# Kernel optimization log

Measured on AMD Instinct MI355X. Metric: run time of the kernel, lower is better.

Reference implementation:

```python
import jax, jax.numpy as jnp
import numpy as np

N_NODES = 100000
N_EDGES = 1600000
IN_CH = 128
HID = 32
HEADS = 4
OUT_CH = 32
NEG_SLOPE = 0.2  # PyG GATConv default


def setup_inputs() -> dict:
    key = jax.random.key(0)
    ks = jax.random.split(key, 12)
    s = 0.1
    x = jax.random.normal(ks[0], (N_NODES, IN_CH), dtype=jnp.float32)
    edge_index = jax.random.randint(ks[1], (2, N_EDGES), 0, N_NODES, dtype=jnp.int64)
    # layer 1: in -> heads*hid, concat
    W1 = jax.random.normal(ks[2], (IN_CH, HEADS * HID), dtype=jnp.float32) * s
    a_src1 = jax.random.normal(ks[3], (HEADS, HID), dtype=jnp.float32) * s
    a_dst1 = jax.random.normal(ks[4], (HEADS, HID), dtype=jnp.float32) * s
    b1 = jnp.zeros((HEADS * HID,), dtype=jnp.float32)
    # layer 2: heads*hid -> out, single head, averaged
    W2 = jax.random.normal(ks[5], (HEADS * HID, OUT_CH), dtype=jnp.float32) * s
    a_src2 = jax.random.normal(ks[6], (1, OUT_CH), dtype=jnp.float32) * s
    a_dst2 = jax.random.normal(ks[7], (1, OUT_CH), dtype=jnp.float32) * s
    b2 = jnp.zeros((OUT_CH,), dtype=jnp.float32)
    return {"x": x, "edge_index": edge_index, "W1": W1, "a_src1": a_src1,
            "a_dst1": a_dst1, "b1": b1, "W2": W2, "a_src2": a_src2,
            "a_dst2": a_dst2, "b2": b2}


def _gat_layer(x, src, dst, W, a_s, a_d, b, heads, ch, concat):
    n = x.shape[0]
    h = (x @ W).reshape(n, heads, ch)            # [N,H,C]
    alpha_s = jnp.einsum('nhc,hc->nh', h, a_s)   # [N,H]
    alpha_d = jnp.einsum('nhc,hc->nh', h, a_d)
    e = jax.nn.leaky_relu(alpha_s[src] + alpha_d[dst], NEG_SLOPE)  # [E,H]
    # segment softmax over edges sharing a destination (self-loops guarantee
    # every segment is non-empty)
    m = jax.ops.segment_max(e, dst, num_segments=n)
    ex = jnp.exp(e - m[dst])
    denom = jax.ops.segment_sum(ex, dst, num_segments=n)
    alpha = ex / (denom[dst] + 1e-16)            # [E,H]
    out = jax.ops.segment_sum(alpha[:, :, None] * h[src], dst, num_segments=n)  # [N,H,C]
    out = out.reshape(n, heads * ch) if concat else out.mean(axis=1)
    return out + b


def reference(x, edge_index, W1, a_src1, a_dst1, b1, W2, a_src2, a_dst2, b2):
    n = x.shape[0]
    loop = jnp.arange(n, dtype=edge_index.dtype)
    src = jnp.concatenate([edge_index[0], loop])  # add self-loops (PyG default)
    dst = jnp.concatenate([edge_index[1], loop])
    h = _gat_layer(x, src, dst, W1, a_src1, a_dst1, b1, HEADS, HID, True)
    h = jax.nn.relu(h)
    # dropout(p=0.5) is identity in eval mode
    out = _gat_layer(h, src, dst, W2, a_src2, a_dst2, b2, 1, OUT_CH, False)
    return out
```

## Files before the change

kernel.cpp:

```cpp
#include <hip/hip_runtime.h>
#include <math.h>

#define NEG_SLOPE 0.2f
#define EPB 8192

typedef __attribute__((ext_vector_type(8))) short bf16x8;
typedef __attribute__((ext_vector_type(4))) float f32x4;

__device__ __forceinline__ unsigned pack_bf16x2(float a, float b) {
    unsigned ua = __float_as_uint(a);
    unsigned ub = __float_as_uint(b);
    ua += 0x7FFFu + ((ua >> 16) & 1u);
    ub += 0x7FFFu + ((ub >> 16) & 1u);
    return (ua >> 16) | (ub & 0xFFFF0000u);
}
__device__ __forceinline__ unsigned short bf16r(float f) {
    unsigned u = __float_as_uint(f);
    u += 0x7FFFu + ((u >> 16) & 1u);
    return (unsigned short)(u >> 16);
}
__device__ __forceinline__ float bf_lo(unsigned u) { return __uint_as_float(u << 16); }
__device__ __forceinline__ float bf_hi(unsigned u) { return __uint_as_float(u & 0xFFFF0000u); }

#define SWZ(row, byteoff) ((((row) * 256) + (byteoff)) ^ (((row) & 15) << 4))


__global__ __launch_bounds__(256) void wcvt_kernel(const float* __restrict__ W,
                                                   unsigned short* __restrict__ WT,
                                                   int Nc, int total) {
    int id = blockIdx.x * 256 + threadIdx.x;
    if (id < total) {
        int n = id >> 7, k = id & 127;
        WT[id] = bf16r(W[k * Nc + n]);
    }
}


__global__ __launch_bounds__(256) void gscan_bsum(const int* __restrict__ arr,
                                                  int* __restrict__ psum, int M) {
    __shared__ int red[4];
    int tid = threadIdx.x;
    int idx = blockIdx.x * 256 + tid;
    int v = (idx < M) ? arr[idx] : 0;
    #pragma unroll
    for (int off = 1; off < 64; off <<= 1) v += __shfl_xor(v, off, 64);
    if ((tid & 63) == 0) red[tid >> 6] = v;
    __syncthreads();
    if (tid == 0) psum[blockIdx.x] = red[0] + red[1] + red[2] + red[3];
}

__global__ __launch_bounds__(1024) void gscan_psum(int* __restrict__ psum, int nb) {
    __shared__ int ws[16];
    int tid = threadIdx.x, lane = tid & 63, w = tid >> 6;
    int v = (tid < nb) ? psum[tid] : 0;
    int incl = v;
    #pragma unroll
    for (int off = 1; off < 64; off <<= 1) {
        int t = __shfl_up(incl, off, 64);
        if (lane >= off) incl += t;
    }
    if (lane == 63) ws[w] = incl;
    __syncthreads();
    int wbase = 0;
    #pragma unroll
    for (int j = 0; j < 16; j++) { if (j < w) wbase += ws[j]; }
    if (tid < nb) psum[tid] = wbase + incl - v;
}

__global__ __launch_bounds__(256) void gscan_final(int* __restrict__ arr,
                                                   const int* __restrict__ psum, int M) {
    __shared__ int ws[4];
    int tid = threadIdx.x, lane = tid & 63, w = tid >> 6;
    int idx = blockIdx.x * 256 + tid;
    int v = (idx < M) ? arr[idx] : 0;
    int incl = v;
    #pragma unroll
    for (int off = 1; off < 64; off <<= 1) {
        int t = __shfl_up(incl, off, 64);
        if (lane >= off) incl += t;
    }
    if (lane == 63) ws[w] = incl;
    __syncthreads();
    int wbase = 0;
    #pragma unroll
    for (int j = 0; j < 4; j++) { if (j < w) wbase += ws[j]; }
    if (idx < M) arr[idx] = psum[blockIdx.x] + wbase + incl - v;
}


__global__ __launch_bounds__(256) void p1_hist(const int* __restrict__ dst, int E, int N,
                                               int nblk1, int nbuckets,
                                               int* __restrict__ partial) {
    __shared__ int hist[1024];
    int tid = threadIdx.x;
    for (int i = tid; i < nbuckets; i += 256) hist[i] = 0;
    __syncthreads();
    int base = blockIdx.x * EPB;
    int tot = E + N;
    #pragma unroll
    for (int it = 0; it < EPB / 256; it++) {
        int i = base + it * 256 + tid;
        if (i < tot) {
            int d = (i < E) ? dst[i] : (i - E);
            atomicAdd(&hist[d >> 8], 1);
        }
    }
    __syncthreads();
    for (int b = tid; b < nbuckets; b += 256)
        partial[b * nblk1 + blockIdx.x] = hist[b];
}

__global__ __launch_bounds__(256) void p1_scatter(const int* __restrict__ src,
                                                  const int* __restrict__ dst, int E, int N,
                                                  int nblk1, int nbuckets,
                                                  const int* __restrict__ scanned,
                                                  unsigned* __restrict__ pairs) {
    __shared__ int cursor[1024];
    int tid = threadIdx.x;
    for (int b = tid; b < nbuckets; b += 256)
        cursor[b] = scanned[b * nblk1 + blockIdx.x];
    __syncthreads();
    int base = blockIdx.x * EPB;
    int tot = E + N;
    #pragma unroll
    for (int it = 0; it < EPB / 256; it++) {
        int i = base + it * 256 + tid;
        if (i < tot) {
            int s = (i < E) ? src[i] : (i - E);
            int d = (i < E) ? dst[i] : (i - E);
            int pos = atomicAdd(&cursor[d >> 8], 1);
            pairs[pos] = ((unsigned)(d & 255) << 24) | (unsigned)s;
        }
    }
}

#define P2CAP 8192

__global__ __launch_bounds__(256) void p2_kernel(const unsigned* __restrict__ pairs,
                                                 const int* __restrict__ scanned,
                                                 int nblk1, int nbuckets, int Etot, int N,
                                                 int* __restrict__ rowptr,
                                                 int* __restrict__ col) {
    __shared__ unsigned buf[P2CAP];
    __shared__ int cnt[256];
    __shared__ int cur[256];
    __shared__ int wsum[4];
    int b = blockIdx.x;
    int tid = threadIdx.x, lane = tid & 63, w = tid >> 6;
    int bucketStart = scanned[b * nblk1];
    int bucketEnd = (b + 1 < nbuckets) ? scanned[(b + 1) * nblk1] : Etot;
    int sz = bucketEnd - bucketStart;
    bool inLds = (sz <= P2CAP);
    cnt[tid] = 0;
    if (inLds) {
        for (int i = tid; i < sz; i += 256) buf[i] = pairs[bucketStart + i];
    }
    __syncthreads();
    if (inLds) {
        for (int i = tid; i < sz; i += 256) atomicAdd(&cnt[buf[i] >> 24], 1);
    } else {
        for (int i = bucketStart + tid; i < bucketEnd; i += 256)
            atomicAdd(&cnt[pairs[i] >> 24], 1);
    }
    __syncthreads();
    int v = cnt[tid];
    int incl = v;
    #pragma unroll
    for (int off = 1; off < 64; off <<= 1) {
        int t = __shfl_up(incl, off, 64);
        if (lane >= off) incl += t;
    }
    if (lane == 63) wsum[w] = incl;
    __syncthreads();
    int wbase = 0;
    #pragma unroll
    for (int j = 0; j < 4; j++) { if (j < w) wbase += wsum[j]; }
    int base = bucketStart + wbase + incl - v;
    cur[tid] = base;
    int d = b * 256 + tid;
    if (d < N) rowptr[d] = base;
    if (b == nbuckets - 1 && tid == 0) rowptr[N] = Etot;
    __syncthreads();
    if (inLds) {
        for (int i = tid; i < sz; i += 256) {
            unsigned p = buf[i];
            int pos = atomicAdd(&cur[p >> 24], 1);
            col[pos] = (int)(p & 0xFFFFFFu);
        }
    } else {
        for (int i = bucketStart + tid; i < bucketEnd; i += 256) {
            unsigned p = pairs[i];
            int pos = atomicAdd(&cur[p >> 24], 1);
            col[pos] = (int)(p & 0xFFFFFFu);
        }
    }
}


__global__ __launch_bounds__(256) void gemm1_kernel(const float* __restrict__ x,
                                                    const unsigned short* __restrict__ W1T,
                                                    const float* __restrict__ a_s,
                                                    const float* __restrict__ a_d,
                                                    uint4* __restrict__ h1b,
                                                    float* __restrict__ as1,
                                                    float* __restrict__ ad1, int N) {
    __shared__ char xs[16384];
    __shared__ char wsm[32768];
    int tid = threadIdx.x;
    int row0 = blockIdx.x * 64;

    #pragma unroll
    for (int it = 0; it < 8; it++) {
        int idx = it * 256 + tid;
        int n = idx >> 4, kq = idx & 15;
        uint4 v = ((const uint4*)W1T)[idx];
        *(uint4*)(wsm + SWZ(n, kq * 16)) = v;
    }
    #pragma unroll
    for (int it = 0; it < 8; it++) {
        int idx = it * 256 + tid;
        int r = idx >> 5, k4 = idx & 31;
        int row = row0 + r;
        float4 v = (row < N) ? ((const float4*)x)[(size_t)row * 32 + k4]
                             : make_float4(0.f, 0.f, 0.f, 0.f);
        uint2 p;
        p.x = pack_bf16x2(v.x, v.y);
        p.y = pack_bf16x2(v.z, v.w);
        *(uint2*)(xs + SWZ(r, k4 * 8)) = p;
    }
    __syncthreads();

    int wv = tid >> 6, lane = tid & 63;
    int r0 = wv * 16;
    int lm = lane & 15, lk = lane >> 4;

    bf16x8 afr[4];
    #pragma unroll
    for (int ks = 0; ks < 4; ks++) {
        int row = r0 + lm;
        afr[ks] = *(const bf16x8*)(xs + SWZ(row, ks * 64 + lk * 16));
    }
    f32x4 acc[8];
    #pragma unroll
    for (int nt = 0; nt < 8; nt++) acc[nt] = (f32x4){0.f, 0.f, 0.f, 0.f};

    #pragma unroll
    for (int nt = 0; nt < 8; nt++) {
        int c = nt * 16 + lm;
        #pragma unroll
        for (int ks = 0; ks < 4; ks++) {
            bf16x8 bfr = *(const bf16x8*)(wsm + SWZ(c, ks * 64 + lk * 16));
            acc[nt] = __builtin_amdgcn_mfma_f32_16x16x32_bf16(afr[ks], bfr, acc[nt], 0, 0, 0);
        }
    }
    __syncthreads();

    #pragma unroll
    for (int nt = 0; nt < 8; nt++) {
        int c = nt * 16 + lm;
        #pragma unroll
        for (int e = 0; e < 4; e++) {
            int row = r0 + lk * 4 + e;
            *(unsigned short*)(xs + SWZ(row, c * 2)) = bf16r(acc[nt][e]);
        }
    }
    __syncthreads();

    #pragma unroll
    for (int it = 0; it < 4; it++) {
        int idx = it * 256 + tid;
        int row = idx >> 4, q = idx & 15;
        if (row0 + row < N) {
            uint4 v = *(const uint4*)(xs + SWZ(row, q * 16));
            h1b[(size_t)(row0 + row) * 16 + q] = v;
        }
    }
    {
        int row = tid >> 2, h = tid & 3;
        if (row0 + row < N) {
            float sd = 0.f, dd = 0.f;
            #pragma unroll
            for (int q = 0; q < 4; q++) {
                uint4 v = *(const uint4*)(xs + SWZ(row, h * 64 + q * 16));
                unsigned uu[4] = {v.x, v.y, v.z, v.w};
                #pragma unroll
                for (int j = 0; j < 4; j++) {
                    int k = h * 32 + q * 8 + 2 * j;
                    sd = fmaf(bf_lo(uu[j]), a_s[k], sd);
                    sd = fmaf(bf_hi(uu[j]), a_s[k + 1], sd);
                    dd = fmaf(bf_lo(uu[j]), a_d[k], dd);
                    dd = fmaf(bf_hi(uu[j]), a_d[k + 1], dd);
                }
            }
            as1[(row0 + row) * 4 + h] = sd;
            ad1[(row0 + row) * 4 + h] = dd;
        }
    }
}


__global__ __launch_bounds__(256) void agg1_kernel(const int* __restrict__ rowptr,
                                                   const int* __restrict__ col,
                                                   const unsigned* __restrict__ h1b,
                                                   const float* __restrict__ as1,
                                                   const float* __restrict__ ad1,
                                                   const float* __restrict__ b1,
                                                   unsigned* __restrict__ out1b, int N) {
    int lane = threadIdx.x & 63;
    int wid = __builtin_amdgcn_readfirstlane(threadIdx.x >> 6);
    int n = blockIdx.x * 4 + wid;
    if (n >= N) return;
    int hh = lane >> 4;
    float adn = ad1[n * 4 + hh];
    int beg = rowptr[n], end = rowptr[n + 1];
    float ax0 = 0.f, ay0 = 0.f, den0 = 0.f;
    float ax1 = 0.f, ay1 = 0.f, den1 = 0.f;
    int i = beg;
    for (; i + 16 <= end; i += 16) {
        int ss[16];
        float ll[16];
        unsigned uu[16];
        #pragma unroll
        for (int j = 0; j < 16; j++) ss[j] = col[i + j];
        #pragma unroll
        for (int j = 0; j < 16; j++) {
            ll[j] = as1[ss[j] * 4 + hh];
            uu[j] = h1b[ss[j] * 64 + lane];
        }
        #pragma unroll
        for (int j = 0; j < 16; j++) {
            float e = ll[j] + adn;
            e = fmaxf(e, e * NEG_SLOPE);
            float ex = __expf(e);
            if (j & 1) {
                den1 += ex;
                ax1 = fmaf(ex, bf_lo(uu[j]), ax1);
                ay1 = fmaf(ex, bf_hi(uu[j]), ay1);
            } else {
                den0 += ex;
                ax0 = fmaf(ex, bf_lo(uu[j]), ax0);
                ay0 = fmaf(ex, bf_hi(uu[j]), ay0);
            }
        }
    }
    for (; i + 4 <= end; i += 4) {
        int ss[4];
        float ll[4];
        unsigned uu[4];
        #pragma unroll
        for (int j = 0; j < 4; j++) ss[j] = col[i + j];
        #pragma unroll
        for (int j = 0; j < 4; j++) {
            ll[j] = as1[ss[j] * 4 + hh];
            uu[j] = h1b[ss[j] * 64 + lane];
        }
        #pragma unroll
        for (int j = 0; j < 4; j++) {
            float e = ll[j] + adn;
            e = fmaxf(e, e * NEG_SLOPE);
            float ex = __expf(e);
            den0 += ex;
            ax0 = fmaf(ex, bf_lo(uu[j]), ax0);
            ay0 = fmaf(ex, bf_hi(uu[j]), ay0);
        }
    }
    for (; i < end; i++) {
        int s = col[i];
        float l = as1[s * 4 + hh];
        unsigned u = h1b[s * 64 + lane];
        float e = l + adn;
        e = fmaxf(e, e * NEG_SLOPE);
        float ex = __expf(e);
        den0 += ex;
        ax0 = fmaf(ex, bf_lo(u), ax0);
        ay0 = fmaf(ex, bf_hi(u), ay0);
    }
    float den = den0 + den1, ax = ax0 + ax1, ay = ay0 + ay1;
    float2 bb = ((const float2*)b1)[lane];
    float ox = fmaxf(ax / den + bb.x, 0.f);
    float oy = fmaxf(ay / den + bb.y, 0.f);
    out1b[n * 64 + lane] = pack_bf16x2(ox, oy);
}


__global__ __launch_bounds__(256) void gemm2_kernel(const uint4* __restrict__ out1b,
                                                    const unsigned short* __restrict__ W2T,
                                                    const float* __restrict__ a_s,
                                                    const float* __restrict__ a_d,
                                                    uint4* __restrict__ h2b,
                                                    float* __restrict__ as2,
                                                    float* __restrict__ ad2, int N) {
    __shared__ char xs[16384];
    __shared__ char wsm[8192];
    int tid = threadIdx.x;
    int row0 = blockIdx.x * 64;

    #pragma unroll
    for (int it = 0; it < 2; it++) {
        int idx = it * 256 + tid;
        int n = idx >> 4, kq = idx & 15;
        uint4 v = ((const uint4*)W2T)[idx];
        *(uint4*)(wsm + SWZ(n, kq * 16)) = v;
    }
    #pragma unroll
    for (int it = 0; it < 4; it++) {
        int idx = it * 256 + tid;
        int r = idx >> 4, q = idx & 15;
        int row = row0 + r;
        uint4 v = (row < N) ? out1b[(size_t)row * 16 + q] : make_uint4(0, 0, 0, 0);
        *(uint4*)(xs + SWZ(r, q * 16)) = v;
    }
    __syncthreads();

    int wv = tid >> 6, lane = tid & 63;
    int r0 = wv * 16;
    int lm = lane & 15, lk = lane >> 4;

    bf16x8 afr[4];
    #pragma unroll
    for (int ks = 0; ks < 4; ks++) {
        int row = r0 + lm;
        afr[ks] = *(const bf16x8*)(xs + SWZ(row, ks * 64 + lk * 16));
    }
    f32x4 acc[2];
    acc[0] = (f32x4){0.f, 0.f, 0.f, 0.f};
    acc[1] = (f32x4){0.f, 0.f, 0.f, 0.f};
    #pragma unroll
    for (int nt = 0; nt < 2; nt++) {
        int c = nt * 16 + lm;
        #pragma unroll
        for (int ks = 0; ks < 4; ks++) {
            bf16x8 bfr = *(const bf16x8*)(wsm + SWZ(c, ks * 64 + lk * 16));
            acc[nt] = __builtin_amdgcn_mfma_f32_16x16x32_bf16(afr[ks], bfr, acc[nt], 0, 0, 0);
        }
    }
    __syncthreads();

    #pragma unroll
    for (int nt = 0; nt < 2; nt++) {
        int c = nt * 16 + lm;
        #pragma unroll
        for (int e = 0; e < 4; e++) {
            int row = r0 + lk * 4 + e;
            *(unsigned short*)(xs + SWZ(row, c * 2)) = bf16r(acc[nt][e]);
        }
    }
    __syncthreads();

    {
        int row = tid >> 2, q = tid & 3;
        if (row0 + row < N) {
            uint4 v = *(const uint4*)(xs + SWZ(row, q * 16));
            h2b[(size_t)(row0 + row) * 4 + q] = v;
        }
    }
    if (tid < 64 && row0 + tid < N) {
        float sd = 0.f, dd = 0.f;
        #pragma unroll
        for (int q = 0; q < 4; q++) {
            uint4 v = *(const uint4*)(xs + SWZ(tid, q * 16));
            unsigned uu[4] = {v.x, v.y, v.z, v.w};
            #pragma unroll
            for (int j = 0; j < 4; j++) {
                int k = q * 8 + 2 * j;
                sd = fmaf(bf_lo(uu[j]), a_s[k], sd);
                sd = fmaf(bf_hi(uu[j]), a_s[k + 1], sd);
                dd = fmaf(bf_lo(uu[j]), a_d[k], dd);
                dd = fmaf(bf_hi(uu[j]), a_d[k + 1], dd);
            }
        }
        as2[row0 + tid] = sd;
        ad2[row0 + tid] = dd;
    }
}


#define AGG2_EDGE(u, l)                                            \
    {                                                              \
        float e = l + adn;                                         \
        e = fmaxf(e, e * NEG_SLOPE);                               \
        float ex = __expf(e);                                      \
        den += ex;                                                 \
        a0 = fmaf(ex, bf_lo(u), a0);                               \
        a1 = fmaf(ex, bf_hi(u), a1);                               \
    }

__global__ __launch_bounds__(256) void agg2_kernel(const int* __restrict__ rowptr,
                                                   const int* __restrict__ col,
                                                   const unsigned* __restrict__ h2b,
                                                   const float* __restrict__ as2,
                                                   const float* __restrict__ ad2,
                                                   const float* __restrict__ b2,
                                                   float* __restrict__ out, int N) {
    int lane = threadIdx.x & 63;
    int wid = __builtin_amdgcn_readfirstlane(threadIdx.x >> 6);
    int n = blockIdx.x * 4 + wid;
    if (n >= N) return;
    int q = lane >> 4, c2 = lane & 15;
    float adn = ad2[n];
    int beg = rowptr[n], end = rowptr[n + 1];
    float a0 = 0.f, a1 = 0.f, den = 0.f;
    int i = beg;
    for (; i + 16 <= end; i += 16) {
        int s0 = col[i + q];
        int s1 = col[i + 4 + q];
        int s2 = col[i + 8 + q];
        int s3 = col[i + 12 + q];
        unsigned u0 = h2b[s0 * 16 + c2];
        unsigned u1 = h2b[s1 * 16 + c2];
        unsigned u2 = h2b[s2 * 16 + c2];
        unsigned u3 = h2b[s3 * 16 + c2];
        float l0 = as2[s0], l1 = as2[s1], l2 = as2[s2], l3 = as2[s3];
        AGG2_EDGE(u0, l0) AGG2_EDGE(u1, l1) AGG2_EDGE(u2, l2) AGG2_EDGE(u3, l3)
    }
    for (; i + 4 <= end; i += 4) {
        int s = col[i + q];
        unsigned u = h2b[s * 16 + c2];
        float l = as2[s];
        AGG2_EDGE(u, l)
    }
    if (i + q < end) {
        int s = col[i + q];
        unsigned u = h2b[s * 16 + c2];
        float l = as2[s];
        AGG2_EDGE(u, l)
    }
    den += __shfl_xor(den, 16, 64);
    den += __shfl_xor(den, 32, 64);
    a0 += __shfl_xor(a0, 16, 64);
    a0 += __shfl_xor(a0, 32, 64);
    a1 += __shfl_xor(a1, 16, 64);
    a1 += __shfl_xor(a1, 32, 64);
    if (q == 0) {
        float2 bb = ((const float2*)b2)[c2];
        ((float2*)out)[n * 16 + c2] = make_float2(a0 / den + bb.x, a1 / den + bb.y);
    }
}


extern "C" void kernel_launch(void* const* d_in, const int* in_sizes, int n_in,
                              void* d_out, int out_size, void* d_ws, size_t ws_size,
                              hipStream_t stream) {
    const float* x    = (const float*)d_in[0];
    const int*   ei   = (const int*)d_in[1];
    const float* W1   = (const float*)d_in[2];
    const float* a_s1 = (const float*)d_in[3];
    const float* a_d1 = (const float*)d_in[4];
    const float* b1   = (const float*)d_in[5];
    const float* W2   = (const float*)d_in[6];
    const float* a_s2 = (const float*)d_in[7];
    const float* a_d2 = (const float*)d_in[8];
    const float* b2   = (const float*)d_in[9];

    int N = in_sizes[0] / 128;
    int E = in_sizes[1] / 2;
    const int* srcA = ei;
    const int* dstA = ei + E;
    int Etot = E + N;

    char* ws = (char*)d_ws;
    size_t off = 0;
    auto alloc = [&](size_t bytes) {
        void* p = ws + off;
        off += (bytes + 255) & ~(size_t)255;
        return p;
    };
    unsigned* h1b   = (unsigned*)alloc((size_t)N * 128 * 2);
    unsigned* out1b = (unsigned*)alloc((size_t)N * 128 * 2);
    unsigned* h2b   = (unsigned*)alloc((size_t)N * 32 * 2);
    float* as1      = (float*)alloc((size_t)N * 4 * 4);
    float* ad1      = (float*)alloc((size_t)N * 4 * 4);
    float* as2      = (float*)alloc((size_t)N * 4);
    float* ad2      = (float*)alloc((size_t)N * 4);
    int*   rowptr   = (int*)alloc((size_t)(N + 1) * 4);
    int*   col      = (int*)alloc((size_t)Etot * 4);
    unsigned* pairs = (unsigned*)alloc((size_t)Etot * 4);
    unsigned short* W1T = (unsigned short*)alloc(128 * 128 * 2);
    unsigned short* W2T = (unsigned short*)alloc(32 * 128 * 2);

    int nbuckets = (N + 255) >> 8;
    int nblk1 = (Etot + EPB - 1) / EPB;
    int M = nbuckets * nblk1;
    int*   partial = (int*)alloc((size_t)M * 4);
    int nbs = (M + 255) / 256;
    int*   psum    = (int*)alloc((size_t)1024 * 4);

    hipLaunchKernelGGL(wcvt_kernel, dim3(64), dim3(256), 0, stream, W1, W1T, 128, 16384);
    hipLaunchKernelGGL(wcvt_kernel, dim3(16), dim3(256), 0, stream, W2, W2T, 32, 4096);

    hipLaunchKernelGGL(p1_hist, dim3(nblk1), dim3(256), 0, stream,
                       dstA, E, N, nblk1, nbuckets, partial);
    hipLaunchKernelGGL(gscan_bsum, dim3(nbs), dim3(256), 0, stream, partial, psum, M);
    hipLaunchKernelGGL(gscan_psum, dim3(1), dim3(1024), 0, stream, psum, nbs);
    hipLaunchKernelGGL(gscan_final, dim3(nbs), dim3(256), 0, stream, partial, psum, M);
    hipLaunchKernelGGL(p1_scatter, dim3(nblk1), dim3(256), 0, stream,
                       srcA, dstA, E, N, nblk1, nbuckets, partial, pairs);
    hipLaunchKernelGGL(p2_kernel, dim3(nbuckets), dim3(256), 0, stream,
                       pairs, partial, nblk1, nbuckets, Etot, N, rowptr, col);

    hipLaunchKernelGGL(gemm1_kernel, dim3((N + 63) / 64), dim3(256), 0, stream,
                       x, W1T, a_s1, a_d1, (uint4*)h1b, as1, ad1, N);
    hipLaunchKernelGGL(agg1_kernel, dim3((N + 3) / 4), dim3(256), 0, stream,
                       rowptr, col, h1b, as1, ad1, b1, out1b, N);
    hipLaunchKernelGGL(gemm2_kernel, dim3((N + 63) / 64), dim3(256), 0, stream,
                       (const uint4*)out1b, W2T, a_s2, a_d2, (uint4*)h2b, as2, ad2, N);
    hipLaunchKernelGGL(agg2_kernel, dim3((N + 3) / 4), dim3(256), 0, stream,
                       rowptr, col, h2b, as2, ad2, b2, (float*)d_out, N);
}
```

Measured before the change: 217.7 us.

## Precompute layer-1 edge attention exponentials in CSR build kernel

Moves gemm1 ahead of the CSR construction so the p2 bucket-sort kernel can compute the leaky-relu and exp of the layer-1 attention logits for all four heads per edge. It writes these into a new per-edge float4 array in CSR order. agg1 then reads the precomputed weights contiguously instead of gathering as1 by source and evaluating exp per lane. This trades a random gather plus exp in agg1 for an extra random as1 gather in p2 and roughly 27 MB of extra edge-array writes and reads.

After: 234.0 us. 7.5% more time.

```diff
diff --git a/kernel.cpp b/kernel.cpp
--- a/kernel.cpp
+++ b/kernel.cpp
@@ -139,8 +139,11 @@
 __global__ __launch_bounds__(256) void p2_kernel(const unsigned* __restrict__ pairs,
                                                  const int* __restrict__ scanned,
                                                  int nblk1, int nbuckets, int Etot, int N,
+                                                 const float4* __restrict__ as4,
+                                                 const float4* __restrict__ ad4,
                                                  int* __restrict__ rowptr,
-                                                 int* __restrict__ col) {
+                                                 int* __restrict__ col,
+                                                 float4* __restrict__ exa) {
     __shared__ unsigned buf[P2CAP];
     __shared__ int cnt[256];
     __shared__ int cur[256];
@@ -184,14 +187,34 @@
     if (inLds) {
         for (int i = tid; i < sz; i += 256) {
             unsigned p = buf[i];
-            int pos = atomicAdd(&cur[p >> 24], 1);
-            col[pos] = (int)(p & 0xFFFFFFu);
+            int dl = p >> 24, s = (int)(p & 0xFFFFFFu);
+            int pos = atomicAdd(&cur[dl], 1);
+            col[pos] = s;
+            float4 A = as4[s];
+            float4 D = ad4[b * 256 + dl];
+            float4 ex;
+            float e;
+            e = A.x + D.x; e = fmaxf(e, e * NEG_SLOPE); ex.x = __expf(e);
+            e = A.y + D.y; e = fmaxf(e, e * NEG_SLOPE); ex.y = __expf(e);
+            e = A.z + D.z; e = fmaxf(e, e * NEG_SLOPE); ex.z = __expf(e);
+            e = A.w + D.w; e = fmaxf(e, e * NEG_SLOPE); ex.w = __expf(e);
+            exa[pos] = ex;
         }
     } else {
         for (int i = bucketStart + tid; i < bucketEnd; i += 256) {
             unsigned p = pairs[i];
-            int pos = atomicAdd(&cur[p >> 24], 1);
-            col[pos] = (int)(p & 0xFFFFFFu);
+            int dl = p >> 24, s = (int)(p & 0xFFFFFFu);
+            int pos = atomicAdd(&cur[dl], 1);
+            col[pos] = s;
+            float4 A = as4[s];
+            float4 D = ad4[b * 256 + dl];
+            float4 ex;
+            float e;
+            e = A.x + D.x; e = fmaxf(e, e * NEG_SLOPE); ex.x = __expf(e);
+            e = A.y + D.y; e = fmaxf(e, e * NEG_SLOPE); ex.y = __expf(e);
+            e = A.z + D.z; e = fmaxf(e, e * NEG_SLOPE); ex.z = __expf(e);
+            e = A.w + D.w; e = fmaxf(e, e * NEG_SLOPE); ex.w = __expf(e);
+            exa[pos] = ex;
         }
     }
 }
@@ -302,8 +325,7 @@
 __global__ __launch_bounds__(256) void agg1_kernel(const int* __restrict__ rowptr,
                                                    const int* __restrict__ col,
                                                    const unsigned* __restrict__ h1b,
-                                                   const float* __restrict__ as1,
-                                                   const float* __restrict__ ad1,
+                                                   const float* __restrict__ exa,
                                                    const float* __restrict__ b1,
                                                    unsigned* __restrict__ out1b, int N) {
     int lane = threadIdx.x & 63;
@@ -311,66 +333,56 @@
     int n = blockIdx.x * 4 + wid;
     if (n >= N) return;
     int hh = lane >> 4;
-    float adn = ad1[n * 4 + hh];
     int beg = rowptr[n], end = rowptr[n + 1];
     float ax0 = 0.f, ay0 = 0.f, den0 = 0.f;
     float ax1 = 0.f, ay1 = 0.f, den1 = 0.f;
     int i = beg;
     for (; i + 16 <= end; i += 16) {
         int ss[16];
-        float ll[16];
+        float ex[16];
         unsigned uu[16];
         #pragma unroll
         for (int j = 0; j < 16; j++) ss[j] = col[i + j];
         #pragma unroll
         for (int j = 0; j < 16; j++) {
-            ll[j] = as1[ss[j] * 4 + hh];
+            ex[j] = exa[(i + j) * 4 + hh];
             uu[j] = h1b[ss[j] * 64 + lane];
         }
         #pragma unroll
         for (int j = 0; j < 16; j++) {
-            float e = ll[j] + adn;
-            e = fmaxf(e, e * NEG_SLOPE);
-            float ex = __expf(e);
             if (j & 1) {
-                den1 += ex;
-                ax1 = fmaf(ex, bf_lo(uu[j]), ax1);
-                ay1 = fmaf(ex, bf_hi(uu[j]), ay1);
+                den1 += ex[j];
+                ax1 = fmaf(ex[j], bf_lo(uu[j]), ax1);
+                ay1 = fmaf(ex[j], bf_hi(uu[j]), ay1);
             } else {
-                den0 += ex;
-                ax0 = fmaf(ex, bf_lo(uu[j]), ax0);
-                ay0 = fmaf(ex, bf_hi(uu[j]), ay0);
+                den0 += ex[j];
+                ax0 = fmaf(ex[j], bf_lo(uu[j]), ax0);
+                ay0 = fmaf(ex[j], bf_hi(uu[j]), ay0);
             }
         }
     }
     for (; i + 4 <= end; i += 4) {
         int ss[4];
-        float ll[4];
+        float ex[4];
         unsigned uu[4];
         #pragma unroll
         for (int j = 0; j < 4; j++) ss[j] = col[i + j];
         #pragma unroll
         for (int j = 0; j < 4; j++) {
-            ll[j] = as1[ss[j] * 4 + hh];
+            ex[j] = exa[(i + j) * 4 + hh];
             uu[j] = h1b[ss[j] * 64 + lane];
         }
         #pragma unroll
         for (int j = 0; j < 4; j++) {
-            float e = ll[j] + adn;
-            e = fmaxf(e, e * NEG_SLOPE);
-            float ex = __expf(e);
-            den0 += ex;
-            ax0 = fmaf(ex, bf_lo(uu[j]), ax0);
-            ay0 = fmaf(ex, bf_hi(uu[j]), ay0);
+            den0 += ex[j];
+            ax0 = fmaf(ex[j], bf_lo(uu[j]), ax0);
+            ay0 = fmaf(ex[j], bf_hi(uu[j]), ay0);
         }
     }
     for (; i < end; i++) {
         int s = col[i];
-        float l = as1[s * 4 + hh];
+        float ex = exa[i * 4 + hh];
         unsigned u = h1b[s * 64 + lane];
-        float e = l + adn;
-        e = fmaxf(e, e * NEG_SLOPE);
-        float ex = __expf(e);
         den0 += ex;
         ax0 = fmaf(ex, bf_lo(u), ax0);
         ay0 = fmaf(ex, bf_hi(u), ay0);
@@ -575,6 +587,7 @@
     int*   rowptr   = (int*)alloc((size_t)(N + 1) * 4);
     int*   col      = (int*)alloc((size_t)Etot * 4);
     unsigned* pairs = (unsigned*)alloc((size_t)Etot * 4);
+    float* exa      = (float*)alloc((size_t)Etot * 16);
     unsigned short* W1T = (unsigned short*)alloc(128 * 128 * 2);
     unsigned short* W2T = (unsigned short*)alloc(32 * 128 * 2);
 
@@ -587,6 +600,8 @@
 
     hipLaunchKernelGGL(wcvt_kernel, dim3(64), dim3(256), 0, stream, W1, W1T, 128, 16384);
     hipLaunchKernelGGL(wcvt_kernel, dim3(16), dim3(256), 0, stream, W2, W2T, 32, 4096);
+    hipLaunchKernelGGL(gemm1_kernel, dim3((N + 63) / 64), dim3(256), 0, stream,
+                       x, W1T, a_s1, a_d1, (uint4*)h1b, as1, ad1, N);
 
     hipLaunchKernelGGL(p1_hist, dim3(nblk1), dim3(256), 0, stream,
                        dstA, E, N, nblk1, nbuckets, partial);
@@ -596,12 +611,11 @@
     hipLaunchKernelGGL(p1_scatter, dim3(nblk1), dim3(256), 0, stream,
                        srcA, dstA, E, N, nblk1, nbuckets, partial, pairs);
     hipLaunchKernelGGL(p2_kernel, dim3(nbuckets), dim3(256), 0, stream,
-                       pairs, partial, nblk1, nbuckets, Etot, N, rowptr, col);
-
-    hipLaunchKernelGGL(gemm1_kernel, dim3((N + 63) / 64), dim3(256), 0, stream,
-                       x, W1T, a_s1, a_d1, (uint4*)h1b, as1, ad1, N);
+                       pairs, partial, nblk1, nbuckets, Etot, N,
+                       (const float4*)as1, (const float4*)ad1, rowptr, col, (float4*)exa);
+
     hipLaunchKernelGGL(agg1_kernel, dim3((N + 3) / 4), dim3(256), 0, stream,
-                       rowptr, col, h1b, as1, ad1, b1, out1b, N);
+                       rowptr, col, h1b, exa, b1, out1b, N);
     hipLaunchKernelGGL(gemm2_kernel, dim3((N + 63) / 64), dim3(256), 0, stream,
                        (const uint4*)out1b, W2T, a_s2, a_d2, (uint4*)h2b, as2, ad2, N);
     hipLaunchKernelGGL(agg2_kernel, dim3((N + 3) / 4), dim3(256), 0, stream,
```

## Precompute layer-1 edge attention exps in separate pass; buffer loads and wider agg2

Applied to the files above, without the earlier changes.

Adds a kernel that computes the per-edge, per-head exp(leaky_relu) attention weights for layer 1 into a head-planar edge array. agg1 then streams these instead of gathering as1 and recomputing exp, and it uses buffer-load intrinsics with four accumulator chains. agg2 is restructured so each lane loads 8 bytes (4 channels) and 8 edges are processed per step. The change also moves gemm1 earlier in the launch order. The cost is an extra kernel launch and roughly 27 MB of extra edge-array write and read traffic, traded for less gather and ALU work inside agg1.

New measurement: 235.0 us. 7.9% more time.

```diff
diff --git a/kernel.cpp b/kernel.cpp
--- a/kernel.cpp
+++ b/kernel.cpp
@@ -21,6 +21,38 @@
 }
 __device__ __forceinline__ float bf_lo(unsigned u) { return __uint_as_float(u << 16); }
 __device__ __forceinline__ float bf_hi(unsigned u) { return __uint_as_float(u & 0xFFFF0000u); }
+
+#if defined(__has_builtin)
+#if __has_builtin(__builtin_amdgcn_make_buffer_rsrc) && \
+    __has_builtin(__builtin_amdgcn_raw_ptr_buffer_load_b32) && \
+    __has_builtin(__builtin_amdgcn_raw_ptr_buffer_load_b64)
+#define USE_BUFLD 1
+#endif
+#endif
+
+#ifdef USE_BUFLD
+typedef __amdgpu_buffer_rsrc_t Rsrc;
+typedef __attribute__((ext_vector_type(2))) unsigned uint2v;
+__device__ __forceinline__ Rsrc mkrsrc(const void* p) {
+    return __builtin_amdgcn_make_buffer_rsrc((void*)p, (short)0, -1, 0x00020000);
+}
+__device__ __forceinline__ unsigned bufld_u32(Rsrc r, int voff) {
+    return __builtin_amdgcn_raw_ptr_buffer_load_b32(r, voff, 0, 0);
+}
+__device__ __forceinline__ float bufld_f32(Rsrc r, int voff) {
+    return __uint_as_float(__builtin_amdgcn_raw_ptr_buffer_load_b32(r, voff, 0, 0));
+}
+__device__ __forceinline__ uint2 bufld_u64(Rsrc r, int voff) {
+    uint2v v = __builtin_amdgcn_raw_ptr_buffer_load_b64(r, voff, 0, 0);
+    return make_uint2(v.x, v.y);
+}
+#else
+struct Rsrc { const char* p; };
+__device__ __forceinline__ Rsrc mkrsrc(const void* p) { Rsrc r; r.p = (const char*)p; return r; }
+__device__ __forceinline__ unsigned bufld_u32(Rsrc r, int voff) { return *(const unsigned*)(r.p + voff); }
+__device__ __forceinline__ float bufld_f32(Rsrc r, int voff) { return *(const float*)(r.p + voff); }
+__device__ __forceinline__ uint2 bufld_u64(Rsrc r, int voff) { return *(const uint2*)(r.p + voff); }
+#endif
 
 #define SWZ(row, byteoff) ((((row) * 256) + (byteoff)) ^ (((row) & 15) << 4))
 
@@ -192,6 +224,34 @@
             unsigned p = pairs[i];
             int pos = atomicAdd(&cur[p >> 24], 1);
             col[pos] = (int)(p & 0xFFFFFFu);
+        }
+    }
+}
+
+
+__global__ __launch_bounds__(256) void exk_kernel(const int* __restrict__ rowptr,
+                                                  const int* __restrict__ col,
+                                                  const float* __restrict__ as1,
+                                                  const float4* __restrict__ ad4,
+                                                  float* __restrict__ exh,
+                                                  int N, int Etot) {
+    int lane = threadIdx.x & 63;
+    int wid = __builtin_amdgcn_readfirstlane(threadIdx.x >> 6);
+    int n = blockIdx.x * 4 + wid;
+    if (n >= N) return;
+    int h = lane >> 4, jj = lane & 15;
+    float4 D = ad4[n];
+    float dn = (h < 2) ? (h == 0 ? D.x : D.y) : (h == 2 ? D.z : D.w);
+    int beg = rowptr[n], end = rowptr[n + 1];
+    int planeBase = h * Etot;
+    for (int i = beg; i < end; i += 16) {
+        int e = i + jj;
+        if (e < end) {
+            int s = col[e];
+            float a = as1[s * 4 + h];
+            float v = a + dn;
+            v = fmaxf(v, v * NEG_SLOPE);
+            exh[planeBase + e] = __expf(v);
         }
     }
 }
@@ -302,80 +362,67 @@
 __global__ __launch_bounds__(256) void agg1_kernel(const int* __restrict__ rowptr,
                                                    const int* __restrict__ col,
                                                    const unsigned* __restrict__ h1b,
-                                                   const float* __restrict__ as1,
-                                                   const float* __restrict__ ad1,
+                                                   const float* __restrict__ exh,
                                                    const float* __restrict__ b1,
-                                                   unsigned* __restrict__ out1b, int N) {
+                                                   unsigned* __restrict__ out1b,
+                                                   int N, int Etot) {
     int lane = threadIdx.x & 63;
     int wid = __builtin_amdgcn_readfirstlane(threadIdx.x >> 6);
     int n = blockIdx.x * 4 + wid;
     if (n >= N) return;
     int hh = lane >> 4;
-    float adn = ad1[n * 4 + hh];
+    Rsrc h1r = mkrsrc(h1b);
+    Rsrc exr = mkrsrc(exh);
+    int laneByte = lane << 2;
+    int exBase = hh * Etot;
     int beg = rowptr[n], end = rowptr[n + 1];
-    float ax0 = 0.f, ay0 = 0.f, den0 = 0.f;
-    float ax1 = 0.f, ay1 = 0.f, den1 = 0.f;
+    float ax0 = 0.f, ay0 = 0.f, d0 = 0.f;
+    float ax1 = 0.f, ay1 = 0.f, d1 = 0.f;
+    float ax2 = 0.f, ay2 = 0.f, d2 = 0.f;
+    float ax3 = 0.f, ay3 = 0.f, d3 = 0.f;
     int i = beg;
     for (; i + 16 <= end; i += 16) {
-        int ss[16];
-        float ll[16];
         unsigned uu[16];
-        #pragma unroll
-        for (int j = 0; j < 16; j++) ss[j] = col[i + j];
+        float ex[16];
         #pragma unroll
         for (int j = 0; j < 16; j++) {
-            ll[j] = as1[ss[j] * 4 + hh];
-            uu[j] = h1b[ss[j] * 64 + lane];
-        }
-        #pragma unroll
-        for (int j = 0; j < 16; j++) {
-            float e = ll[j] + adn;
-            e = fmaxf(e, e * NEG_SLOPE);
-            float ex = __expf(e);
-            if (j & 1) {
-                den1 += ex;
-                ax1 = fmaf(ex, bf_lo(uu[j]), ax1);
-                ay1 = fmaf(ex, bf_hi(uu[j]), ay1);
-            } else {
-                den0 += ex;
-                ax0 = fmaf(ex, bf_lo(uu[j]), ax0);
-                ay0 = fmaf(ex, bf_hi(uu[j]), ay0);
-            }
+            int s = col[i + j];
+            uu[j] = bufld_u32(h1r, (s << 8) + laneByte);
+            ex[j] = bufld_f32(exr, (exBase + i + j) << 2);
+        }
+        #pragma unroll
+        for (int j = 0; j < 16; j += 4) {
+            d0 += ex[j];     ax0 = fmaf(ex[j],     bf_lo(uu[j]),     ax0); ay0 = fmaf(ex[j],     bf_hi(uu[j]),     ay0);
+            d1 += ex[j + 1]; ax1 = fmaf(ex[j + 1], bf_lo(uu[j + 1]), ax1); ay1 = fmaf(ex[j + 1], bf_hi(uu[j + 1]), ay1);
+            d2 += ex[j + 2]; ax2 = fmaf(ex[j + 2], bf_lo(uu[j + 2]), ax2); ay2 = fmaf(ex[j + 2], bf_hi(uu[j + 2]), ay2);
+            d3 += ex[j + 3]; ax3 = fmaf(ex[j + 3], bf_lo(uu[j + 3]), ax3); ay3 = fmaf(ex[j + 3], bf_hi(uu[j + 3]), ay3);
         }
     }
     for (; i + 4 <= end; i += 4) {
-        int ss[4];
-        float ll[4];
         unsigned uu[4];
-        #pragma unroll
-        for (int j = 0; j < 4; j++) ss[j] = col[i + j];
+        float ex[4];
         #pragma unroll
         for (int j = 0; j < 4; j++) {
-            ll[j] = as1[ss[j] * 4 + hh];
-            uu[j] = h1b[ss[j] * 64 + lane];
-        }
-        #pragma unroll
-        for (int j = 0; j < 4; j++) {
-            float e = ll[j] + adn;
-            e = fmaxf(e, e * NEG_SLOPE);
-            float ex = __expf(e);
-            den0 += ex;
-            ax0 = fmaf(ex, bf_lo(uu[j]), ax0);
-            ay0 = fmaf(ex, bf_hi(uu[j]), ay0);
-        }
+            int s = col[i + j];
+            uu[j] = bufld_u32(h1r, (s << 8) + laneByte);
+            ex[j] = bufld_f32(exr, (exBase + i + j) << 2);
+        }
+        d0 += ex[0]; ax0 = fmaf(ex[0], bf_lo(uu[0]), ax0); ay0 = fmaf(ex[0], bf_hi(uu[0]), ay0);
+        d1 += ex[1]; ax1 = fmaf(ex[1], bf_lo(uu[1]), ax1); ay1 = fmaf(ex[1], bf_hi(uu[1]), ay1);
+        d2 += ex[2]; ax2 = fmaf(ex[2], bf_lo(uu[2]), ax2); ay2 = fmaf(ex[2], bf_hi(uu[2]), ay2);
+        d3 += ex[3]; ax3 = fmaf(ex[3], bf_lo(uu[3]), ax3); ay3 = fmaf(ex[3], bf_hi(uu[3]), ay3);
     }
     for (; i < end; i++) {
         int s = col[i];
-        float l = as1[s * 4 + hh];
-        unsigned u = h1b[s * 64 + lane];
-        float e = l + adn;
-        e = fmaxf(e, e * NEG_SLOPE);
-        float ex = __expf(e);
-        den0 += ex;
-        ax0 = fmaf(ex, bf_lo(u), ax0);
-        ay0 = fmaf(ex, bf_hi(u), ay0);
-    }
-    float den = den0 + den1, ax = ax0 + ax1, ay = ay0 + ay1;
+        unsigned u = bufld_u32(h1r, (s << 8) + laneByte);
+        float x = bufld_f32(exr, (exBase + i) << 2);
+        d0 += x;
+        ax0 = fmaf(x, bf_lo(u), ax0);
+        ay0 = fmaf(x, bf_hi(u), ay0);
+    }
+    float den = (d0 + d1) + (d2 + d3);
+    float ax = (ax0 + ax1) + (ax2 + ax3);
+    float ay = (ay0 + ay1) + (ay2 + ay3);
     float2 bb = ((const float2*)b1)[lane];
     float ox = fmaxf(ax / den + bb.x, 0.f);
     float oy = fmaxf(ay / den + bb.y, 0.f);
@@ -475,14 +522,16 @@
 }
 
 
-#define AGG2_EDGE(u, l)                                            \
+#define A2SLOT(u, l)                                               \
     {                                                              \
         float e = l + adn;                                         \
         e = fmaxf(e, e * NEG_SLOPE);                               \
         float ex = __expf(e);                                      \
         den += ex;                                                 \
-        a0 = fmaf(ex, bf_lo(u), a0);                               \
-        a1 = fmaf(ex, bf_hi(u), a1);                               \
+        a0 = fmaf(ex, bf_lo(u.x), a0);                             \
+        a1 = fmaf(ex, bf_hi(u.x), a1);                             \
+        a2 = fmaf(ex, bf_lo(u.y), a2);                             \
+        a3 = fmaf(ex, bf_hi(u.y), a3);                             \
     }
 
 __global__ __launch_bounds__(256) void agg2_kernel(const int* __restrict__ rowptr,
@@ -496,44 +545,48 @@
     int wid = __builtin_amdgcn_readfirstlane(threadIdx.x >> 6);
     int n = blockIdx.x * 4 + wid;
     if (n >= N) return;
-    int q = lane >> 4, c2 = lane & 15;
+    int q8 = lane >> 3;
+    int cl = lane & 7;
+    Rsrc h2r = mkrsrc(h2b);
+    Rsrc asr = mkrsrc(as2);
+    int clByte = cl << 3;
     float adn = ad2[n];
     int beg = rowptr[n], end = rowptr[n + 1];
-    float a0 = 0.f, a1 = 0.f, den = 0.f;
+    float a0 = 0.f, a1 = 0.f, a2 = 0.f, a3 = 0.f, den = 0.f;
     int i = beg;
     for (; i + 16 <= end; i += 16) {
-        int s0 = col[i + q];
-        int s1 = col[i + 4 + q];
-        int s2 = col[i + 8 + q];
-        int s3 = col[i + 12 + q];
-        unsigned u0 = h2b[s0 * 16 + c2];
-        unsigned u1 = h2b[s1 * 16 + c2];
-        unsigned u2 = h2b[s2 * 16 + c2];
-        unsigned u3 = h2b[s3 * 16 + c2];
-        float l0 = as2[s0], l1 = as2[s1], l2 = as2[s2], l3 = as2[s3];
-        AGG2_EDGE(u0, l0) AGG2_EDGE(u1, l1) AGG2_EDGE(u2, l2) AGG2_EDGE(u3, l3)
-    }
-    for (; i + 4 <= end; i += 4) {
-        int s = col[i + q];
-        unsigned u = h2b[s * 16 + c2];
-        float l = as2[s];
-        AGG2_EDGE(u, l)
-    }
-    if (i + q < end) {
-        int s = col[i + q];
-        unsigned u = h2b[s * 16 + c2];
-        float l = as2[s];
-        AGG2_EDGE(u, l)
-    }
+        int e0 = i + q8, e1 = i + 8 + q8;
+        int s0 = col[e0], s1 = col[e1];
+        uint2 u0 = bufld_u64(h2r, (s0 << 6) + clByte);
+        uint2 u1 = bufld_u64(h2r, (s1 << 6) + clByte);
+        float l0 = bufld_f32(asr, s0 << 2);
+        float l1 = bufld_f32(asr, s1 << 2);
+        A2SLOT(u0, l0) A2SLOT(u1, l1)
+    }
+    for (; i < end; i += 8) {
+        int e = i + q8;
+        if (e < end) {
+            int s = col[e];
+            uint2 u = bufld_u64(h2r, (s << 6) + clByte);
+            float l = bufld_f32(asr, s << 2);
+            A2SLOT(u, l)
+        }
+    }
+    den += __shfl_xor(den, 8, 64);
     den += __shfl_xor(den, 16, 64);
     den += __shfl_xor(den, 32, 64);
-    a0 += __shfl_xor(a0, 16, 64);
-    a0 += __shfl_xor(a0, 32, 64);
-    a1 += __shfl_xor(a1, 16, 64);
-    a1 += __shfl_xor(a1, 32, 64);
-    if (q == 0) {
-        float2 bb = ((const float2*)b2)[c2];
-        ((float2*)out)[n * 16 + c2] = make_float2(a0 / den + bb.x, a1 / den + bb.y);
+    a0 += __shfl_xor(a0, 8, 64);  a0 += __shfl_xor(a0, 16, 64);  a0 += __shfl_xor(a0, 32, 64);
+    a1 += __shfl_xor(a1, 8, 64);  a1 += __shfl_xor(a1, 16, 64);  a1 += __shfl_xor(a1, 32, 64);
+    a2 += __shfl_xor(a2, 8, 64);  a2 += __shfl_xor(a2, 16, 64);  a2 += __shfl_xor(a2, 32, 64);
+    a3 += __shfl_xor(a3, 8, 64);  a3 += __shfl_xor(a3, 16, 64);  a3 += __shfl_xor(a3, 32, 64);
+    if (q8 == 0) {
+        float4 bb = ((const float4*)b2)[cl];
+        float4 o;
+        o.x = a0 / den + bb.x;
+        o.y = a1 / den + bb.y;
+        o.z = a2 / den + bb.z;
+        o.w = a3 / den + bb.w;
+        ((float4*)out)[n * 8 + cl] = o;
     }
 }
 
@@ -575,6 +628,7 @@
     int*   rowptr   = (int*)alloc((size_t)(N + 1) * 4);
     int*   col      = (int*)alloc((size_t)Etot * 4);
     unsigned* pairs = (unsigned*)alloc((size_t)Etot * 4);
+    float* exh      = (float*)alloc((size_t)Etot * 4 * 4);
     unsigned short* W1T = (unsigned short*)alloc(128 * 128 * 2);
     unsigned short* W2T = (unsigned short*)alloc(32 * 128 * 2);
 
@@ -587,6 +641,8 @@
 
     hipLaunchKernelGGL(wcvt_kernel, dim3(64), dim3(256), 0, stream, W1, W1T, 128, 16384);
     hipLaunchKernelGGL(wcvt_kernel, dim3(16), dim3(256), 0, stream, W2, W2T, 32, 4096);
+    hipLaunchKernelGGL(gemm1_kernel, dim3((N + 63) / 64), dim3(256), 0, stream,
+                       x, W1T, a_s1, a_d1, (uint4*)h1b, as1, ad1, N);
 
     hipLaunchKernelGGL(p1_hist, dim3(nblk1), dim3(256), 0, stream,
                        dstA, E, N, nblk1, nbuckets, partial);
@@ -598,10 +654,11 @@
     hipLaunchKernelGGL(p2_kernel, dim3(nbuckets), dim3(256), 0, stream,
                        pairs, partial, nblk1, nbuckets, Etot, N, rowptr, col);
 
-    hipLaunchKernelGGL(gemm1_kernel, dim3((N + 63) / 64), dim3(256), 0, stream,
-                       x, W1T, a_s1, a_d1, (uint4*)h1b, as1, ad1, N);
+    hipLaunchKernelGGL(exk_kernel, dim3((N + 3) / 4), dim3(256), 0, stream,
+                       rowptr, col, as1, (const float4*)ad1, exh, N, Etot);
+
     hipLaunchKernelGGL(agg1_kernel, dim3((N + 3) / 4), dim3(256), 0, stream,
-                       rowptr, col, h1b, as1, ad1, b1, out1b, N);
+                       rowptr, col, h1b, exh, b1, out1b, N, Etot);
     hipLaunchKernelGGL(gemm2_kernel, dim3((N + 63) / 64), dim3(256), 0, stream,
                        (const uint4*)out1b, W2T, a_s2, a_d2, (uint4*)h2b, as2, ad2, N);
     hipLaunchKernelGGL(agg2_kernel, dim3((N + 3) / 4), dim3(256), 0, stream,
```
